# Optimization experiments

Measured on AMD Instinct MI355X. Metric: run time of the kernel, lower is better.

## Reference

```python
import jax, jax.numpy as jnp
import numpy as np

B, S, D, N, L, V = 4, 2048, 512, 16, 4, 256
EPS = 1e-5


def layernorm(x, g, b):
    m = x.mean(-1, keepdims=True)
    v = ((x - m) ** 2).mean(-1, keepdims=True)
    return (x - m) * jax.lax.rsqrt(v + EPS) * g + b


def ssm_layer(x, logA, Wd, bd, WB, bB, WC, bC, WDp, bDp, g, be):
    # x: (B,S,D)
    h = layernorm(x, g, be)
    delta = jax.nn.softplus(h @ Wd + bd)          # (B,S,D)
    Bi = h @ WB + bB                              # (B,S,N)
    Ci = h @ WC + bC                              # (B,S,N)
    A = -jnp.exp(logA)                            # (D,N)

    def step(state, inp):
        d_t, b_t, c_t, h_t = inp                  # (B,D),(B,N),(B,N),(B,D)
        dA = jnp.exp(d_t[:, :, None] * A)         # (B,D,N)
        state = dA * state + (d_t * h_t)[:, :, None] * b_t[:, None, :]
        y_t = jnp.einsum('bdn,bn->bd', state, c_t)
        return state, y_t

    xs = (jnp.moveaxis(delta, 1, 0), jnp.moveaxis(Bi, 1, 0),
          jnp.moveaxis(Ci, 1, 0), jnp.moveaxis(h, 1, 0))
    init = jnp.zeros((x.shape[0], x.shape[2], logA.shape[-1]), x.dtype)
    _, ys = jax.lax.scan(step, init, xs)
    y = jnp.moveaxis(ys, 0, 1)                    # (B,S,D)
    return x + y + h @ WDp + bDp


def setup_inputs() -> dict:
    key = jax.random.key(0)
    ks = jax.random.split(key, 12)
    s = 0.02
    byte_ids = jax.random.randint(ks[0], (B, S), 0, 256)
    emb_byte = jax.random.normal(ks[1], (V, D), jnp.float32) * s
    emb_pos = jax.random.normal(ks[2], (S, D), jnp.float32) * s
    logA = jnp.tile(jnp.log(jnp.linspace(1.0, N, N, dtype=jnp.float32)), (L, D, 1))
    Wd = jax.random.normal(ks[3], (L, D, D), jnp.float32) * s
    bd = jnp.zeros((L, D), jnp.float32)
    WB = jax.random.normal(ks[4], (L, D, N), jnp.float32) * s
    bB = jnp.zeros((L, N), jnp.float32)
    WC = jax.random.normal(ks[5], (L, D, N), jnp.float32) * s
    bC = jnp.zeros((L, N), jnp.float32)
    WDp = jax.random.normal(ks[6], (L, D, D), jnp.float32) * s
    bDp = jnp.zeros((L, D), jnp.float32)
    gamma = jnp.ones((L, D), jnp.float32)
    beta = jnp.zeros((L, D), jnp.float32)
    Wh = jax.random.normal(ks[7], (D, V), jnp.float32) * s
    bh = jnp.zeros((V,), jnp.float32)
    return {'byte_ids': byte_ids, 'emb_byte': emb_byte, 'emb_pos': emb_pos,
            'logA': logA, 'Wd': Wd, 'bd': bd, 'WB': WB, 'bB': bB,
            'WC': WC, 'bC': bC, 'WDp': WDp, 'bDp': bDp,
            'gamma': gamma, 'beta': beta, 'Wh': Wh, 'bh': bh}


def reference(byte_ids, emb_byte, emb_pos, logA, Wd, bd, WB, bB, WC, bC,
              WDp, bDp, gamma, beta, Wh, bh):
    S_ = byte_ids.shape[1]
    h = emb_byte[byte_ids] + emb_pos[:S_]
    for l in range(Wd.shape[0]):
        h = ssm_layer(h, logA[l], Wd[l], bd[l], WB[l], bB[l], WC[l], bC[l],
                      WDp[l], bDp[l], gamma[l], beta[l])
    return h @ Wh + bh                            # (B,S,256) logits
```

## Files before the change

### kernel.cpp

```cpp
#include <hip/hip_runtime.h>
#include <math.h>

#define BB 4
#define SS 2048
#define DD 512
#define NN 16
#define LL 4
#define VV 256
#define CC 128
#define TT (SS / CC)
#define EPSL 1e-5f
#define MM (BB * SS)
#define KI 16
#define LPAD 528

typedef __bf16 bf16;
typedef __attribute__((ext_vector_type(8))) __bf16 bf16x8;
typedef __attribute__((ext_vector_type(4))) __bf16 bf16x4;
typedef __attribute__((ext_vector_type(4))) float f32x4;


#define GLD_LDS(g, l) \
    __builtin_amdgcn_global_load_lds((__attribute__((address_space(1))) void*)(void*)(g), \
                                     (__attribute__((address_space(3))) void*)(l), 16, 0, 0)

__device__ __forceinline__ void ln_row_write(float4 v0, float4 v1, int lane, size_t row,
                                             const float* __restrict__ gamma,
                                             const float* __restrict__ beta,
                                             float* HN, bf16* HNb) {
    float s = v0.x + v0.y + v0.z + v0.w + v1.x + v1.y + v1.z + v1.w;
    float q = v0.x * v0.x + v0.y * v0.y + v0.z * v0.z + v0.w * v0.w +
              v1.x * v1.x + v1.y * v1.y + v1.z * v1.z + v1.w * v1.w;
#pragma unroll
    for (int o = 1; o < 64; o <<= 1) {
        s += __shfl_xor(s, o);
        q += __shfl_xor(q, o);
    }
    float m = s * (1.0f / DD);
    float var = q * (1.0f / DD) - m * m;
    float rs = rsqrtf(var + EPSL);
    float4 g0 = *(const float4*)(gamma + lane * 4);
    float4 g1 = *(const float4*)(gamma + 256 + lane * 4);
    float4 b0 = *(const float4*)(beta + lane * 4);
    float4 b1 = *(const float4*)(beta + 256 + lane * 4);
    float4 o0, o1;
    o0.x = (v0.x - m) * rs * g0.x + b0.x;
    o0.y = (v0.y - m) * rs * g0.y + b0.y;
    o0.z = (v0.z - m) * rs * g0.z + b0.z;
    o0.w = (v0.w - m) * rs * g0.w + b0.w;
    o1.x = (v1.x - m) * rs * g1.x + b1.x;
    o1.y = (v1.y - m) * rs * g1.y + b1.y;
    o1.z = (v1.z - m) * rs * g1.z + b1.z;
    o1.w = (v1.w - m) * rs * g1.w + b1.w;
    float* hr = HN + row * DD;
    *(float4*)(hr + lane * 4) = o0;
    *(float4*)(hr + 256 + lane * 4) = o1;
    size_t pb = (size_t)(row >> 4) * 8192 + (size_t)(lane >> 3) * 512 +
                (size_t)((lane & 7) >> 1) * 128 + (row & 15) * 8 + (lane & 1) * 4;
    bf16x4 p0 = {(bf16)o0.x, (bf16)o0.y, (bf16)o0.z, (bf16)o0.w};
    bf16x4 p1 = {(bf16)o1.x, (bf16)o1.y, (bf16)o1.z, (bf16)o1.w};
    *(bf16x4*)(HNb + pb) = p0;
    *(bf16x4*)(HNb + pb + 8 * 512) = p1;
}

__global__ void embed_ln(const int* __restrict__ ids,
                         const float* __restrict__ eb,
                         const float* __restrict__ ep,
                         const float* __restrict__ gamma,
                         const float* __restrict__ beta,
                         float* __restrict__ X, float* HN, bf16* HNb) {
    int wave = threadIdx.x >> 6;
    int lane = threadIdx.x & 63;
    size_t row = blockIdx.x * 4 + wave;
    int s = (int)(row & (SS - 1));
    int id = ids[row];
    const float* ebr = eb + (size_t)id * DD;
    const float* epr = ep + (size_t)s * DD;
    float4 e0 = *(const float4*)(ebr + lane * 4);
    float4 e1 = *(const float4*)(ebr + 256 + lane * 4);
    float4 p0 = *(const float4*)(epr + lane * 4);
    float4 p1 = *(const float4*)(epr + 256 + lane * 4);
    float4 v0 = {e0.x + p0.x, e0.y + p0.y, e0.z + p0.z, e0.w + p0.w};
    float4 v1 = {e1.x + p1.x, e1.y + p1.y, e1.z + p1.z, e1.w + p1.w};
    *(float4*)(X + row * DD + lane * 4) = v0;
    *(float4*)(X + row * DD + 256 + lane * 4) = v1;
    ln_row_write(v0, v1, lane, row, gamma, beta, HN, HNb);
}

__global__ __launch_bounds__(256) void convert_weights(const float* __restrict__ Wd,
                                                       const float* __restrict__ WDp,
                                                       const float* __restrict__ Wh,
                                                       bf16* __restrict__ WtP) {
    __shared__ float slab[512 * 17];
    int blk = blockIdx.x;
    const float* src;
    int nsrc, col0;
    bf16* dst;
    if (blk < 256) {
        int l = blk >> 6, tile = blk & 63;
        src = (tile < 32) ? (Wd + (size_t)l * DD * DD) : (WDp + (size_t)l * DD * DD);
        col0 = (tile & 31) * 16;
        nsrc = DD;
        dst = WtP + ((size_t)l * 64 + tile) * 8192;
    } else {
        int tile = blk - 256;
        src = Wh;
        col0 = tile * 16;
        nsrc = VV;
        dst = WtP + (size_t)(256 + tile) * 8192;
    }
    int tid = threadIdx.x;
    int kr = tid >> 2, cq = tid & 3;
#pragma unroll
    for (int i = 0; i < 8; i++) {
        int k = i * 64 + kr;
        float4 v = *(const float4*)(src + (size_t)k * nsrc + col0 + cq * 4);
        slab[k * 17 + cq * 4 + 0] = v.x;
        slab[k * 17 + cq * 4 + 1] = v.y;
        slab[k * 17 + cq * 4 + 2] = v.z;
        slab[k * 17 + cq * 4 + 3] = v.w;
    }
    __syncthreads();
#pragma unroll
    for (int it = 0; it < 4; it++) {
        int c = it * 256 + tid;
        int ki = c >> 6, fq = (c >> 4) & 3, fm = c & 15;
        int k0 = ki * 32 + fq * 8;
        bf16x8 v;
#pragma unroll
        for (int e = 0; e < 8; e++) v[e] = (bf16)slab[(k0 + e) * 17 + fm];
        *(bf16x8*)(dst + (size_t)c * 8) = v;
    }
}

template <int MODE, int NT>
__global__ __launch_bounds__(256, 8) void gemm_pack(const bf16* __restrict__ Ap,
                                                    const bf16* __restrict__ Bp,
                                                    const float* __restrict__ bias,
                                                    const float* __restrict__ bias2,
                                                    const float* __restrict__ Xres,
                                                    float* __restrict__ O1,
                                                    float* __restrict__ O2, int Nout) {
    __shared__ bf16 As[4 * 512];
    __shared__ bf16 Bs[4 * 512];
    const int tid = threadIdx.x, wave = tid >> 6, lane = tid & 63;
    const int lin = blockIdx.x;
    const int xcd = lin & 7, i4 = lin >> 3;
    const int ms = xcd * 16 + (i4 & 15);
    const int nb = i4 >> 4;

    const bf16* gA = Ap + ((size_t)ms * 4 + wave) * 8192 + lane * 8;
    const bf16* gB = Bp + ((size_t)nb * 4 + wave) * 8192 + lane * 8;
    bf16* lA = As + wave * 512;
    bf16* lB = Bs + wave * 512;

    const int fa0 = (wave >> 1) * 2, fb0 = (wave & 1) * 2;

    f32x4 acc[2][2];
#pragma unroll
    for (int i = 0; i < 2; i++)
#pragma unroll
        for (int j = 0; j < 2; j++) acc[i][j] = (f32x4){0.f, 0.f, 0.f, 0.f};

    for (int ki = 0; ki < KI; ki++) {
        GLD_LDS(gA + ki * 512, lA);
        GLD_LDS(gB + ki * 512, lB);
        __syncthreads();
        bf16x8 af[2], bfr[2];
#pragma unroll
        for (int i = 0; i < 2; i++) af[i] = *(const bf16x8*)(As + (fa0 + i) * 512 + lane * 8);
#pragma unroll
        for (int j = 0; j < 2; j++) bfr[j] = *(const bf16x8*)(Bs + (fb0 + j) * 512 + lane * 8);
#pragma unroll
        for (int i = 0; i < 2; i++)
#pragma unroll
            for (int j = 0; j < 2; j++)
                acc[i][j] = __builtin_amdgcn_mfma_f32_16x16x32_bf16(af[i], bfr[j], acc[i][j], 0, 0, 0);
        __syncthreads();
    }

    const int fm = lane & 15, fq = lane >> 4;
#pragma unroll
    for (int i = 0; i < 2; i++) {
#pragma unroll
        for (int j = 0; j < 2; j++) {
            int col = (nb * 4 + fb0 + j) * 16 + fm;
#pragma unroll
            for (int r = 0; r < 4; r++) {
                int row = (ms * 4 + fa0 + i) * 16 + fq * 4 + r;
                float v = acc[i][j][r];
                if (MODE == 0) {
                    O1[(size_t)row * Nout + col] = v + bias[col];
                } else {
                    if (col < DD) {
                        v += bias[col];
                        v = fmaxf(v, 0.0f) + log1pf(__expf(-fabsf(v)));
                        O1[(size_t)row * DD + col] = v;
                    } else {
                        int c = col - DD;
                        O2[(size_t)row * DD + c] = v + bias2[c] + Xres[(size_t)row * DD + c];
                    }
                }
            }
        }
    }
}

__global__ __launch_bounds__(256) void bcproj(const float* __restrict__ HN,
                                              const float* __restrict__ WB,
                                              const float* __restrict__ bB,
                                              const float* __restrict__ WC,
                                              const float* __restrict__ bC,
                                              float* __restrict__ BIo,
                                              float* __restrict__ CIo) {
    __shared__ float W[512 * 32];
    int tid = threadIdx.x;
#pragma unroll
    for (int i = 0; i < 8; i++) {
        int f = i * 256 + tid;
        int k = f >> 2, c4 = (f & 3) * 4;
        float4 v = *(const float4*)(WB + (size_t)f * 4);
        W[k * 32 + c4 + 0] = v.x;
        W[k * 32 + c4 + 1] = v.y;
        W[k * 32 + c4 + 2] = v.z;
        W[k * 32 + c4 + 3] = v.w;
        float4 u = *(const float4*)(WC + (size_t)f * 4);
        W[k * 32 + 16 + c4 + 0] = u.x;
        W[k * 32 + 16 + c4 + 1] = u.y;
        W[k * 32 + 16 + c4 + 2] = u.z;
        W[k * 32 + 16 + c4 + 3] = u.w;
    }
    __syncthreads();
    int r = tid >> 5, c = tid & 31;
    size_t row = (size_t)blockIdx.x * 8 + r;
    const float* hr = HN + row * DD;
    float acc0 = 0.0f, acc1 = 0.0f;
#pragma unroll 4
    for (int k = 0; k < DD; k += 8) {
        float4 a0 = *(const float4*)(hr + k);
        float4 a1 = *(const float4*)(hr + k + 4);
        acc0 = fmaf(a0.x, W[(k + 0) * 32 + c], acc0);
        acc1 = fmaf(a0.y, W[(k + 1) * 32 + c], acc1);
        acc0 = fmaf(a0.z, W[(k + 2) * 32 + c], acc0);
        acc1 = fmaf(a0.w, W[(k + 3) * 32 + c], acc1);
        acc0 = fmaf(a1.x, W[(k + 4) * 32 + c], acc0);
        acc1 = fmaf(a1.y, W[(k + 5) * 32 + c], acc1);
        acc0 = fmaf(a1.z, W[(k + 6) * 32 + c], acc0);
        acc1 = fmaf(a1.w, W[(k + 7) * 32 + c], acc1);
    }
    float acc = acc0 + acc1;
    if (c < NN) BIo[row * NN + c] = acc + bB[c];
    else        CIo[row * NN + (c - NN)] = acc + bC[c - NN];
}

__global__ __launch_bounds__(512) void scan1(const float* __restrict__ DEL,
                                             const float* __restrict__ HN,
                                             const float* __restrict__ BIc,
                                             const float* __restrict__ logA,
                                             float* __restrict__ P,
                                             float* __restrict__ LSt) {
    __shared__ float bis[TT * NN];
    int b = blockIdx.x >> 7, c = blockIdx.x & (CC - 1);
    int d = threadIdx.x;
    size_t row0 = (size_t)b * SS + (size_t)c * TT;
    if (d < TT * NN) bis[d] = BIc[row0 * NN + d];
    float Ar[NN], prod[NN], st[NN];
    const float* la = logA + d * NN;
#pragma unroll
    for (int n = 0; n < NN; n += 4) {
        float4 a4 = *(const float4*)(la + n);
        Ar[n + 0] = -__expf(a4.x);
        Ar[n + 1] = -__expf(a4.y);
        Ar[n + 2] = -__expf(a4.z);
        Ar[n + 3] = -__expf(a4.w);
    }
#pragma unroll
    for (int n = 0; n < NN; n++) {
        prod[n] = 1.0f;
        st[n] = 0.0f;
    }
    __syncthreads();
    const float* dp = DEL + row0 * DD + d;
    const float* hp = HN + row0 * DD + d;
#pragma unroll 4
    for (int tt = 0; tt < TT; tt++) {
        float dl = dp[(size_t)tt * DD];
        float du = dl * hp[(size_t)tt * DD];
#pragma unroll
        for (int n = 0; n < NN; n++) {
            float a = __expf(dl * Ar[n]);
            prod[n] *= a;
            st[n] = fmaf(a, st[n], du * bis[tt * NN + n]);
        }
    }
    size_t o = (((size_t)b * CC + c) * DD + d) * NN;
#pragma unroll
    for (int n = 0; n < NN; n += 4) {
        *(f32x4*)(P + o + n) = (f32x4){prod[n], prod[n + 1], prod[n + 2], prod[n + 3]};
        *(f32x4*)(LSt + o + n) = (f32x4){st[n], st[n + 1], st[n + 2], st[n + 3]};
    }
}

__global__ __launch_bounds__(256) void scan2(const float* __restrict__ P,
                                             float* __restrict__ LS) {
    __shared__ float sP[256], sL[256];
    int bd = blockIdx.x;
    int b = bd >> 9, d = bd & (DD - 1);
    int n = threadIdx.x & (NN - 1), g = threadIdx.x >> 4;
    size_t base = ((size_t)b * CC * DD + d) * NN + n;
    const size_t cs = (size_t)DD * NN;
    float p[8], l[8];
#pragma unroll
    for (int i = 0; i < 8; i++) {
        size_t o = base + (size_t)(g * 8 + i) * cs;
        p[i] = P[o];
        l[i] = LS[o];
    }
    float FP = 1.0f, FL = 0.0f;
#pragma unroll
    for (int i = 0; i < 8; i++) {
        FL = fmaf(p[i], FL, l[i]);
        FP *= p[i];
    }
    sP[threadIdx.x] = FP;
    sL[threadIdx.x] = FL;
    __syncthreads();
    if (threadIdx.x < NN) {
        int nn = threadIdx.x;
        float s = 0.0f;
#pragma unroll
        for (int gg = 0; gg < 16; gg++) {
            float fp = sP[gg * 16 + nn];
            float fl = sL[gg * 16 + nn];
            sL[gg * 16 + nn] = s;
            s = fmaf(fp, s, fl);
        }
    }
    __syncthreads();
    float s = sL[g * 16 + n];
#pragma unroll
    for (int i = 0; i < 8; i++) {
        size_t o = base + (size_t)(g * 8 + i) * cs;
        LS[o] = s;
        s = fmaf(p[i], s, l[i]);
    }
}

template <int LAST>
__global__ __launch_bounds__(512) void scan3ln(const float* __restrict__ DEL,
                                               float* HN,
                                               const float* __restrict__ BI,
                                               const float* __restrict__ CI,
                                               const float* __restrict__ logA,
                                               const float* __restrict__ SIN,
                                               const float* __restrict__ D2,
                                               const float* __restrict__ gamma,
                                               const float* __restrict__ beta,
                                               float* __restrict__ X,
                                               bf16* HNb) {
    __shared__ float xvs[TT * LPAD];
    __shared__ float bis[TT * NN], cis[TT * NN];
    int b = blockIdx.x >> 7, c = blockIdx.x & (CC - 1);
    int d = threadIdx.x;
    size_t row0 = (size_t)b * SS + (size_t)c * TT;
    if (d < TT * NN) {
        bis[d] = BI[row0 * NN + d];
        cis[d] = CI[row0 * NN + d];
    }
    float Ar[NN], st[NN];
    size_t o = (((size_t)b * CC + c) * DD + d) * NN;
    const float* la = logA + d * NN;
#pragma unroll
    for (int n = 0; n < NN; n += 4) {
        float4 a4 = *(const float4*)(la + n);
        Ar[n + 0] = -__expf(a4.x);
        Ar[n + 1] = -__expf(a4.y);
        Ar[n + 2] = -__expf(a4.z);
        Ar[n + 3] = -__expf(a4.w);
        float4 s4 = *(const float4*)(SIN + o + n);
        st[n + 0] = s4.x;
        st[n + 1] = s4.y;
        st[n + 2] = s4.z;
        st[n + 3] = s4.w;
    }
    __syncthreads();
    const float* dp = DEL + row0 * DD + d;
    const float* hp = HN + row0 * DD + d;
    const float* d2p = D2 + row0 * DD + d;
    float* xp = X + row0 * DD + d;
#pragma unroll 4
    for (int tt = 0; tt < TT; tt++) {
        float dl = dp[(size_t)tt * DD];
        float du = dl * hp[(size_t)tt * DD];
        float y = 0.0f;
#pragma unroll
        for (int n = 0; n < NN; n++) {
            float a = __expf(dl * Ar[n]);
            st[n] = fmaf(a, st[n], du * bis[tt * NN + n]);
            y = fmaf(st[n], cis[tt * NN + n], y);
        }
        float xv = d2p[(size_t)tt * DD] + y;
        xvs[tt * LPAD + d] = xv;
        if (!LAST) xp[(size_t)tt * DD] = xv;
    }
    __syncthreads();
    int wv = d >> 6, lane = d & 63;
#pragma unroll
    for (int r = 0; r < 2; r++) {
        int tt = wv * 2 + r;
        size_t row = row0 + tt;
        const float* xr = xvs + tt * LPAD;
        float4 v0 = *(const float4*)(xr + lane * 4);
        float4 v1 = *(const float4*)(xr + 256 + lane * 4);
        if (LAST) {
            size_t pb = (size_t)(row >> 4) * 8192 + (size_t)(lane >> 3) * 512 +
                        (size_t)((lane & 7) >> 1) * 128 + (row & 15) * 8 + (lane & 1) * 4;
            bf16x4 p0 = {(bf16)v0.x, (bf16)v0.y, (bf16)v0.z, (bf16)v0.w};
            bf16x4 p1 = {(bf16)v1.x, (bf16)v1.y, (bf16)v1.z, (bf16)v1.w};
            *(bf16x4*)(HNb + pb) = p0;
            *(bf16x4*)(HNb + pb + 8 * 512) = p1;
        } else {
            ln_row_write(v0, v1, lane, row, gamma, beta, HN, HNb);
        }
    }
}

extern "C" void kernel_launch(void* const* d_in, const int* in_sizes, int n_in,
                              void* d_out, int out_size, void* d_ws, size_t ws_size,
                              hipStream_t stream) {
    const int* ids = (const int*)d_in[0];
    const float* eb = (const float*)d_in[1];
    const float* ep = (const float*)d_in[2];
    const float* logA = (const float*)d_in[3];
    const float* Wd = (const float*)d_in[4];
    const float* bd = (const float*)d_in[5];
    const float* WB = (const float*)d_in[6];
    const float* bB = (const float*)d_in[7];
    const float* WC = (const float*)d_in[8];
    const float* bC = (const float*)d_in[9];
    const float* WDp = (const float*)d_in[10];
    const float* bDp = (const float*)d_in[11];
    const float* gamma = (const float*)d_in[12];
    const float* beta = (const float*)d_in[13];
    const float* Wh = (const float*)d_in[14];
    const float* bh = (const float*)d_in[15];
    float* out = (float*)d_out;

    size_t E = (size_t)MM * DD;
    size_t EN = (size_t)MM * NN;
    float* X = (float*)d_ws;
    float* HN = X + E;
    float* DEL = HN + E;
    float* D2 = DEL + E;
    float* LS = D2 + E;
    bf16* HNb = (bf16*)(LS + E);
    bf16* WtP = HNb + E;
    float* P = X;
    float* BIc = out;
    float* CIc = out + EN;

    embed_ln<<<MM / 4, 256, 0, stream>>>(ids, eb, ep, gamma, beta, X, HN, HNb);
    convert_weights<<<272, 256, 0, stream>>>(Wd, WDp, Wh, WtP);
    for (int l = 0; l < LL; l++) {
        const float* lA = logA + (size_t)l * DD * NN;
        bcproj<<<MM / 8, 256, 0, stream>>>(HN, WB + (size_t)l * DD * NN, bB + l * NN,
                                           WC + (size_t)l * DD * NN, bC + l * NN,
                                           BIc, CIc);
        gemm_pack<1, 16><<<2048, 256, 0, stream>>>(
            HNb, WtP + (size_t)l * 524288, bd + l * DD, bDp + l * DD, X, DEL, D2, 1024);
        scan1<<<BB * CC, 512, 0, stream>>>(DEL, HN, BIc, lA, P, LS);
        scan2<<<BB * DD, 256, 0, stream>>>(P, LS);
        if (l < LL - 1) {
            scan3ln<0><<<BB * CC, 512, 0, stream>>>(DEL, HN, BIc, CIc, lA, LS, D2,
                                                    gamma + (l + 1) * DD, beta + (l + 1) * DD,
                                                    X, HNb);
        } else {
            scan3ln<1><<<BB * CC, 512, 0, stream>>>(DEL, HN, BIc, CIc, lA, LS, D2,
                                                    nullptr, nullptr, X, HNb);
        }
    }
    gemm_pack<0, 4><<<512, 256, 0, stream>>>(
        HNb, WtP + (size_t)2097152, bh, nullptr, nullptr, out, nullptr, VV);
}
```

Baseline: 544.8 us.

## Enlarge GEMM tiles to 128x128, register-block bcproj rows, replace scan1 product with exp-sum

Both GEMM paths now use a larger block tile: 8 A and 8 B fragment slabs per block, with each wave computing a 4x4 grid of MFMA fragments instead of 2x2. This raises data reuse per LDS load and launches fewer blocks. The B/C projection kernel now has each thread compute four rows at a time, so each LDS weight read is reused across those rows. In scan1, the per-step running product of decay factors is replaced by a single exponential of the accumulated delta sum, removing 16 multiplies per step. The larger tiles reduce parallelism (512 and 128 blocks) and raise register pressure, and the XCD-aware block mapping is dropped.

```diff
diff --git a/kernel.cpp b/kernel.cpp
--- a/kernel.cpp
+++ b/kernel.cpp
@@ -133,61 +133,66 @@
     }
 }
 
-template <int MODE, int NT>
-__global__ __launch_bounds__(256, 8) void gemm_pack(const bf16* __restrict__ Ap,
-                                                    const bf16* __restrict__ Bp,
-                                                    const float* __restrict__ bias,
-                                                    const float* __restrict__ bias2,
-                                                    const float* __restrict__ Xres,
-                                                    float* __restrict__ O1,
-                                                    float* __restrict__ O2, int Nout) {
-    __shared__ bf16 As[4 * 512];
-    __shared__ bf16 Bs[4 * 512];
+template <int MODE, int NB>
+__global__ __launch_bounds__(256) void gemm128(const bf16* __restrict__ Ap,
+                                               const bf16* __restrict__ Bp,
+                                               const float* __restrict__ bias,
+                                               const float* __restrict__ bias2,
+                                               const float* __restrict__ Xres,
+                                               float* __restrict__ O1,
+                                               float* __restrict__ O2, int Nout) {
+    __shared__ bf16 As[8 * 512];
+    __shared__ bf16 Bs[8 * 512];
     const int tid = threadIdx.x, wave = tid >> 6, lane = tid & 63;
-    const int lin = blockIdx.x;
-    const int xcd = lin & 7, i4 = lin >> 3;
-    const int ms = xcd * 16 + (i4 & 15);
-    const int nb = i4 >> 4;
-
-    const bf16* gA = Ap + ((size_t)ms * 4 + wave) * 8192 + lane * 8;
-    const bf16* gB = Bp + ((size_t)nb * 4 + wave) * 8192 + lane * 8;
-    bf16* lA = As + wave * 512;
-    bf16* lB = Bs + wave * 512;
-
-    const int fa0 = (wave >> 1) * 2, fb0 = (wave & 1) * 2;
-
-    f32x4 acc[2][2];
-#pragma unroll
-    for (int i = 0; i < 2; i++)
-#pragma unroll
-        for (int j = 0; j < 2; j++) acc[i][j] = (f32x4){0.f, 0.f, 0.f, 0.f};
+    const int nb = blockIdx.x >> 6;
+    const int ms = blockIdx.x & 63;
+    const int wr = wave >> 1, wc = wave & 1;
+
+    const bf16* gA0 = Ap + ((size_t)ms * 8 + wave) * 8192 + lane * 8;
+    const bf16* gA1 = gA0 + (size_t)4 * 8192;
+    const bf16* gB0 = Bp + ((size_t)nb * 8 + wave) * 8192 + lane * 8;
+    const bf16* gB1 = gB0 + (size_t)4 * 8192;
+    bf16* lA0 = As + wave * 512;
+    bf16* lA1 = As + (wave + 4) * 512;
+    bf16* lB0 = Bs + wave * 512;
+    bf16* lB1 = Bs + (wave + 4) * 512;
+
+    f32x4 acc[4][4];
+#pragma unroll
+    for (int i = 0; i < 4; i++)
+#pragma unroll
+        for (int j = 0; j < 4; j++) acc[i][j] = (f32x4){0.f, 0.f, 0.f, 0.f};
 
     for (int ki = 0; ki < KI; ki++) {
-        GLD_LDS(gA + ki * 512, lA);
-        GLD_LDS(gB + ki * 512, lB);
+        GLD_LDS(gA0 + ki * 512, lA0);
+        GLD_LDS(gA1 + ki * 512, lA1);
+        GLD_LDS(gB0 + ki * 512, lB0);
+        GLD_LDS(gB1 + ki * 512, lB1);
         __syncthreads();
-        bf16x8 af[2], bfr[2];
-#pragma unroll
-        for (int i = 0; i < 2; i++) af[i] = *(const bf16x8*)(As + (fa0 + i) * 512 + lane * 8);
-#pragma unroll
-        for (int j = 0; j < 2; j++) bfr[j] = *(const bf16x8*)(Bs + (fb0 + j) * 512 + lane * 8);
-#pragma unroll
-        for (int i = 0; i < 2; i++)
-#pragma unroll
-            for (int j = 0; j < 2; j++)
+        bf16x8 af[4], bfr[4];
+#pragma unroll
+        for (int i = 0; i < 4; i++)
+            af[i] = *(const bf16x8*)(As + (wr * 4 + i) * 512 + lane * 8);
+#pragma unroll
+        for (int j = 0; j < 4; j++)
+            bfr[j] = *(const bf16x8*)(Bs + (wc * 4 + j) * 512 + lane * 8);
+#pragma unroll
+        for (int i = 0; i < 4; i++)
+#pragma unroll
+            for (int j = 0; j < 4; j++)
                 acc[i][j] = __builtin_amdgcn_mfma_f32_16x16x32_bf16(af[i], bfr[j], acc[i][j], 0, 0, 0);
         __syncthreads();
     }
 
     const int fm = lane & 15, fq = lane >> 4;
 #pragma unroll
-    for (int i = 0; i < 2; i++) {
-#pragma unroll
-        for (int j = 0; j < 2; j++) {
-            int col = (nb * 4 + fb0 + j) * 16 + fm;
+    for (int i = 0; i < 4; i++) {
+#pragma unroll
+        for (int j = 0; j < 4; j++) {
+            int col = (nb * 8 + wc * 4 + j) * 16 + fm;
 #pragma unroll
             for (int r = 0; r < 4; r++) {
-                int row = (ms * 4 + fa0 + i) * 16 + fq * 4 + r;
+                int row = (ms * 8 + wr * 4 + i) * 16 + fq * 4 + r;
                 float v = acc[i][j][r];
                 if (MODE == 0) {
                     O1[(size_t)row * Nout + col] = v + bias[col];
@@ -231,26 +236,46 @@
         W[k * 32 + 16 + c4 + 3] = u.w;
     }
     __syncthreads();
-    int r = tid >> 5, c = tid & 31;
-    size_t row = (size_t)blockIdx.x * 8 + r;
-    const float* hr = HN + row * DD;
-    float acc0 = 0.0f, acc1 = 0.0f;
+    int rg = tid >> 5, c = tid & 31;
+    size_t row0 = (size_t)blockIdx.x * 32 + rg * 4;
+    const float* h0 = HN + row0 * DD;
+    const float* h1 = h0 + DD;
+    const float* h2 = h1 + DD;
+    const float* h3 = h2 + DD;
+    float a0 = 0.f, a1 = 0.f, a2 = 0.f, a3 = 0.f;
 #pragma unroll 4
-    for (int k = 0; k < DD; k += 8) {
-        float4 a0 = *(const float4*)(hr + k);
-        float4 a1 = *(const float4*)(hr + k + 4);
-        acc0 = fmaf(a0.x, W[(k + 0) * 32 + c], acc0);
-        acc1 = fmaf(a0.y, W[(k + 1) * 32 + c], acc1);
-        acc0 = fmaf(a0.z, W[(k + 2) * 32 + c], acc0);
-        acc1 = fmaf(a0.w, W[(k + 3) * 32 + c], acc1);
-        acc0 = fmaf(a1.x, W[(k + 4) * 32 + c], acc0);
-        acc1 = fmaf(a1.y, W[(k + 5) * 32 + c], acc1);
-        acc0 = fmaf(a1.z, W[(k + 6) * 32 + c], acc0);
-        acc1 = fmaf(a1.w, W[(k + 7) * 32 + c], acc1);
-    }
-    float acc = acc0 + acc1;
-    if (c < NN) BIo[row * NN + c] = acc + bB[c];
-    else        CIo[row * NN + (c - NN)] = acc + bC[c - NN];
+    for (int k = 0; k < DD; k += 4) {
+        float4 v0 = *(const float4*)(h0 + k);
+        float4 v1 = *(const float4*)(h1 + k);
+        float4 v2 = *(const float4*)(h2 + k);
+        float4 v3 = *(const float4*)(h3 + k);
+        float w0 = W[(k + 0) * 32 + c];
+        float w1 = W[(k + 1) * 32 + c];
+        float w2 = W[(k + 2) * 32 + c];
+        float w3 = W[(k + 3) * 32 + c];
+        a0 = fmaf(v0.x, w0, a0); a0 = fmaf(v0.y, w1, a0);
+        a0 = fmaf(v0.z, w2, a0); a0 = fmaf(v0.w, w3, a0);
+        a1 = fmaf(v1.x, w0, a1); a1 = fmaf(v1.y, w1, a1);
+        a1 = fmaf(v1.z, w2, a1); a1 = fmaf(v1.w, w3, a1);
+        a2 = fmaf(v2.x, w0, a2); a2 = fmaf(v2.y, w1, a2);
+        a2 = fmaf(v2.z, w2, a2); a2 = fmaf(v2.w, w3, a2);
+        a3 = fmaf(v3.x, w0, a3); a3 = fmaf(v3.y, w1, a3);
+        a3 = fmaf(v3.z, w2, a3); a3 = fmaf(v3.w, w3, a3);
+    }
+    if (c < NN) {
+        float bb = bB[c];
+        BIo[(row0 + 0) * NN + c] = a0 + bb;
+        BIo[(row0 + 1) * NN + c] = a1 + bb;
+        BIo[(row0 + 2) * NN + c] = a2 + bb;
+        BIo[(row0 + 3) * NN + c] = a3 + bb;
+    } else {
+        int cc = c - NN;
+        float bb = bC[cc];
+        CIo[(row0 + 0) * NN + cc] = a0 + bb;
+        CIo[(row0 + 1) * NN + cc] = a1 + bb;
+        CIo[(row0 + 2) * NN + cc] = a2 + bb;
+        CIo[(row0 + 3) * NN + cc] = a3 + bb;
+    }
 }
 
 __global__ __launch_bounds__(512) void scan1(const float* __restrict__ DEL,
@@ -264,7 +289,7 @@
     int d = threadIdx.x;
     size_t row0 = (size_t)b * SS + (size_t)c * TT;
     if (d < TT * NN) bis[d] = BIc[row0 * NN + d];
-    float Ar[NN], prod[NN], st[NN];
+    float Ar[NN], st[NN];
     const float* la = logA + d * NN;
 #pragma unroll
     for (int n = 0; n < NN; n += 4) {
@@ -275,10 +300,8 @@
         Ar[n + 3] = -__expf(a4.w);
     }
 #pragma unroll
-    for (int n = 0; n < NN; n++) {
-        prod[n] = 1.0f;
-        st[n] = 0.0f;
-    }
+    for (int n = 0; n < NN; n++) st[n] = 0.0f;
+    float sdl = 0.0f;
     __syncthreads();
     const float* dp = DEL + row0 * DD + d;
     const float* hp = HN + row0 * DD + d;
@@ -286,17 +309,18 @@
     for (int tt = 0; tt < TT; tt++) {
         float dl = dp[(size_t)tt * DD];
         float du = dl * hp[(size_t)tt * DD];
+        sdl += dl;
 #pragma unroll
         for (int n = 0; n < NN; n++) {
             float a = __expf(dl * Ar[n]);
-            prod[n] *= a;
             st[n] = fmaf(a, st[n], du * bis[tt * NN + n]);
         }
     }
     size_t o = (((size_t)b * CC + c) * DD + d) * NN;
 #pragma unroll
     for (int n = 0; n < NN; n += 4) {
-        *(f32x4*)(P + o + n) = (f32x4){prod[n], prod[n + 1], prod[n + 2], prod[n + 3]};
+        *(f32x4*)(P + o + n) = (f32x4){__expf(Ar[n] * sdl), __expf(Ar[n + 1] * sdl),
+                                       __expf(Ar[n + 2] * sdl), __expf(Ar[n + 3] * sdl)};
         *(f32x4*)(LSt + o + n) = (f32x4){st[n], st[n + 1], st[n + 2], st[n + 3]};
     }
 }
@@ -463,10 +487,10 @@
     convert_weights<<<272, 256, 0, stream>>>(Wd, WDp, Wh, WtP);
     for (int l = 0; l < LL; l++) {
         const float* lA = logA + (size_t)l * DD * NN;
-        bcproj<<<MM / 8, 256, 0, stream>>>(HN, WB + (size_t)l * DD * NN, bB + l * NN,
-                                           WC + (size_t)l * DD * NN, bC + l * NN,
-                                           BIc, CIc);
-        gemm_pack<1, 16><<<2048, 256, 0, stream>>>(
+        bcproj<<<MM / 32, 256, 0, stream>>>(HN, WB + (size_t)l * DD * NN, bB + l * NN,
+                                            WC + (size_t)l * DD * NN, bC + l * NN,
+                                            BIc, CIc);
+        gemm128<1, 8><<<512, 256, 0, stream>>>(
             HNb, WtP + (size_t)l * 524288, bd + l * DD, bDp + l * DD, X, DEL, D2, 1024);
         scan1<<<BB * CC, 512, 0, stream>>>(DEL, HN, BIc, lA, P, LS);
         scan2<<<BB * DD, 256, 0, stream>>>(P, LS);
@@ -479,6 +503,6 @@
                                                     nullptr, nullptr, X, HNb);
         }
     }
-    gemm_pack<0, 4><<<512, 256, 0, stream>>>(
+    gemm128<0, 2><<<128, 256, 0, stream>>>(
         HNb, WtP + (size_t)2097152, bh, nullptr, nullptr, out, nullptr, VV);
 }
```

Result: slower. 625.9 us (+14.9%).
